# Performance work log

Measured on AMD Instinct MI355X. Metric: run time of the kernel, lower is better.

Reference implementation:

```python
import jax, jax.numpy as jnp
import numpy as np
from jax import lax

B, T, CIN, FN, H, W = 8, 8, 64, 64, 32, 32
GROUPS = 4 * FN // 32  # 8


def group_norm(x, g, b, groups, eps=1e-5):
    Bn, C, Hh, Ww = x.shape
    xr = x.reshape(Bn, groups, C // groups, Hh, Ww)
    mu = xr.mean(axis=(2, 3, 4), keepdims=True)
    var = xr.var(axis=(2, 3, 4), keepdims=True)
    xn = ((xr - mu) * lax.rsqrt(var + eps)).reshape(Bn, C, Hh, Ww)
    return xn * g[None, :, None, None] + b[None, :, None, None]


def conv1x1(x, w, b):
    # x: [B,C,H,W], w: [O,C]
    return jnp.einsum('bchw,oc->bohw', x, w) + b[None, :, None, None]


def setup_inputs() -> dict:
    key = jax.random.key(0)
    ks = jax.random.split(key, 8)
    s = 0.05
    return {
        'inputs': jax.random.normal(ks[0], (B, T, CIN, H, W), jnp.float32),
        'conv_w': jax.random.normal(ks[1], (4 * FN, CIN + FN, 3, 3), jnp.float32) * s,
        'conv_b': jnp.zeros((4 * FN,), jnp.float32),
        'gn_g': jnp.ones((4 * FN,), jnp.float32),
        'gn_b': jnp.zeros((4 * FN,), jnp.float32),
        'h_w': jax.random.normal(ks[2], (3 * FN, FN), jnp.float32) * s,
        'h_b': jnp.zeros((3 * FN,), jnp.float32),
        'm_w': jax.random.normal(ks[3], (2 * FN, FN), jnp.float32) * s,
        'm_b': jnp.zeros((2 * FN,), jnp.float32),
        'z1_w': jax.random.normal(ks[4], (FN, 2 * FN), jnp.float32) * s,
        'z1_b': jnp.zeros((FN,), jnp.float32),
        'z2_w': jax.random.normal(ks[5], (3 * FN, 2 * FN), jnp.float32) * s,
        'z2_b': jnp.zeros((3 * FN,), jnp.float32),
    }


def _sam(oh, im, h_w, h_b, m_w, m_b, z1_w, z1_b, z2_w, z2_b):
    Bn, C, Hh, Ww = oh.shape
    HW = Hh * Ww
    h_qkv = conv1x1(oh, h_w, h_b)  # [B,3C,H,W]
    m_kv = conv1x1(im, m_w, m_b)   # [B,2C,H,W]
    Qh, Kh, Vh = jnp.split(h_qkv, 3, axis=1)
    Km, Vm = jnp.split(m_kv, 2, axis=1)
    Q = Qh.reshape(Bn, C, HW).transpose(0, 2, 1)  # [B,HW,C]
    Kh = Kh.reshape(Bn, C, HW)
    Vh = Vh.reshape(Bn, C, HW)
    Km = Km.reshape(Bn, C, HW)
    Vm = Vm.reshape(Bn, C, HW)
    Ah = jax.nn.softmax(jnp.einsum('bnc,bcm->bnm', Q, Kh), axis=-1)  # [B,HW,HW]
    Am = jax.nn.softmax(jnp.einsum('bnc,bcm->bnm', Q, Km), axis=-1)
    Zh = jnp.einsum('bcn,bnm->bcm', Vh, Ah)  # [B,C,HW]
    Zm = jnp.einsum('bcn,bnm->bcm', Vm, Am)
    Zcat = jnp.concatenate([Zh, Zm], axis=1).reshape(Bn, 2 * C, Hh, Ww)
    Z = conv1x1(Zcat, z1_w, z1_b)  # [B,C,H,W]
    gates = conv1x1(jnp.concatenate([Z, oh], axis=1), z2_w, z2_b)  # [B,3C,H,W]
    o, g, i = jnp.split(gates, 3, axis=1)
    i = jax.nn.sigmoid(i)
    om = jnp.tanh(g) * i + (1.0 - i) * im
    oh2 = jax.nn.sigmoid(o) * om
    return oh2, om


def reference(inputs, conv_w, conv_b, gn_g, gn_b, h_w, h_b, m_w, m_b, z1_w, z1_b, z2_w, z2_b):
    Bn = inputs.shape[0]
    Hh, Ww = inputs.shape[-2], inputs.shape[-1]
    ih0 = jnp.zeros((Bn, FN, Hh, Ww), inputs.dtype)
    ic0 = jnp.zeros_like(ih0)
    im0 = jnp.zeros_like(ih0)

    def step(carry, x):
        ih, ic, im = carry
        comb = jnp.concatenate([x, ih], axis=1)
        gates = lax.conv_general_dilated(
            comb, conv_w, window_strides=(1, 1), padding='SAME',
            dimension_numbers=('NCHW', 'OIHW', 'NCHW')) + conv_b[None, :, None, None]
        gates = group_norm(gates, gn_g, gn_b, GROUPS)
        ingate, forgetgate, cellgate, outgate = jnp.split(gates, 4, axis=1)
        oc = ic * jax.nn.sigmoid(forgetgate) + jax.nn.sigmoid(ingate) * jnp.tanh(cellgate)
        oh = jax.nn.sigmoid(outgate) * jnp.tanh(oc)
        oh, om = _sam(oh, im, h_w, h_b, m_w, m_b, z1_w, z1_b, z2_w, z2_b)
        return (oh, oc, om), oh

    xs = jnp.moveaxis(inputs, 1, 0)  # [T,B,C,H,W]
    (ohT, ocT, imT), ys = lax.scan(step, (ih0, ic0, im0), xs)
    out = jnp.moveaxis(ys, 0, 1)  # [B,T,FN,H,W]
    return out, (ohT, ocT, imT)
```

## Files before the change

kernel.cpp:

```cpp
#include <hip/hip_runtime.h>
#include <math.h>


#define DEV __device__ __forceinline__

DEV float sigm(float x) { return 1.0f / (1.0f + __expf(-x)); }

DEV unsigned short f2bf(float f) {
  union { float f; unsigned u; } v; v.f = f;
  unsigned r = v.u + 0x7FFF + ((v.u >> 16) & 1);
  return (unsigned short)(r >> 16);
}

DEV unsigned pk2(float a, float b) {
  return (unsigned)f2bf(a) | ((unsigned)f2bf(b) << 16);
}

typedef float f32x4 __attribute__((ext_vector_type(4)));
typedef short bf16x8 __attribute__((ext_vector_type(8)));

__global__ __launch_bounds__(256) void wprep_kernel(
    const float* __restrict__ w, unsigned short* __restrict__ wpack)
{
  int e = blockIdx.x * 256 + threadIdx.x;
  int ci = e % 40;   int r = e / 40;
  int ocl = r % 128; r /= 128;
  int s = r % 36;    int oh = r / 36;
  int chh = s / 18;
  int t2  = s % 18;
  int tap = t2 >> 1, kc = t2 & 1;
  unsigned short v = 0;
  if (ci < 32) {
    int oc = oh * 128 + ocl;
    int c  = chh * 64 + kc * 32 + ci;
    v = f2bf(w[(size_t)(oc * 128 + c) * 9 + tap]);
  }
  wpack[e] = v;
}

__global__ __launch_bounds__(256) void wproj_kernel(
    const float* __restrict__ h_w, const float* __restrict__ m_w,
    const float* __restrict__ z1_w, const float* __restrict__ z2_w,
    unsigned short* __restrict__ wp)
{
  int e = blockIdx.x * 256 + threadIdx.x;
  if (e >= 53248) return;
  float v;
  if (e < 12288)       v = h_w[e];
  else if (e < 20480)  v = m_w[e - 12288];
  else if (e < 28672)  v = z1_w[e - 20480];
  else                 v = z2_w[e - 28672];
  wp[e] = f2bf(v);
}

__global__ __launch_bounds__(256) void conv3_mfma_kernel(
    const float* __restrict__ x,
    const float* __restrict__ ihb,
    const unsigned short* __restrict__ wpack,
    const float* __restrict__ bias,
    float* __restrict__ gates, int t)
{
  int ptile = blockIdx.x;
  int b     = blockIdx.y;
  int oh    = blockIdx.z;

  __shared__ __align__(16) unsigned short img[4 * 34 * 136];
  __shared__ __align__(16) unsigned short wbuf[2][128 * 40];

  int tid  = threadIdx.x;
  int lane = tid & 63;
  int wv   = tid >> 6;
  int mrow = wv >> 1, ncol = wv & 1;
  int y0 = ptile * 2;

  for (int i = tid; i < 4 * 34 * 136 / 2; i += 256) ((unsigned*)img)[i] = 0u;
  __syncthreads();

  const float* xsrc = x + (size_t)(b * 8 + t) * 65536;
  const float* hsrc = ihb + (size_t)b * 65536;
#pragma unroll
  for (int i = 0; i < 16; ++i) {
    int u = tid + i * 256;
    int ch = u >> 5;
    int v5 = u & 31;
    int row = v5 >> 3;
    int col4 = (v5 & 7) * 4;
    int gy = y0 - 1 + row;
    if (gy >= 0 && gy < 32) {
      const float* src = (ch < 64) ? (xsrc + (size_t)ch * 1024)
                                   : (hsrc + (size_t)(ch - 64) * 1024);
      float4 f = *(const float4*)(src + gy * 32 + col4);
      int base = (row * 34 + col4 + 1) * 136 + ch;
      img[base]       = f2bf(f.x);
      img[base + 136] = f2bf(f.y);
      img[base + 272] = f2bf(f.z);
      img[base + 408] = f2bf(f.w);
    }
  }

  const unsigned* wsl = (const unsigned*)wpack + (size_t)oh * 36 * 2560;
  unsigned* wb32 = (unsigned*)&wbuf[0][0];
#pragma unroll
  for (int k2 = 0; k2 < 10; ++k2)
    wb32[tid + k2 * 256] = wsl[tid + k2 * 256];
  __syncthreads();

  int aoff = (mrow * 64 + (lane & 15)) * 40 + (lane >> 4) * 8;
  int pb[2];
#pragma unroll
  for (int nf = 0; nf < 2; ++nf) {
    int pp = ncol * 32 + nf * 16 + (lane & 15);
    int rr = pp >> 5, cc = pp & 31;
    pb[nf] = (rr * 34 + cc) * 136 + (lane >> 4) * 8;
  }

  f32x4 acc[4][2] = {};
  unsigned wreg[10];

#pragma unroll
  for (int s = 0; s < 36; ++s) {
    int cur = s & 1;
    if (s < 35) {
      const unsigned* nsl = wsl + (s + 1) * 2560;
#pragma unroll
      for (int k2 = 0; k2 < 10; ++k2) wreg[k2] = nsl[tid + k2 * 256];
    }
    int chh = s / 18;
    int t2  = s % 18;
    int tap = t2 >> 1, kc = t2 & 1;
    int dy = tap / 3, dx = tap % 3;
    int toff = (dy * 34 + dx) * 136 + chh * 64 + kc * 32;

    bf16x8 a[4], bb[2];
#pragma unroll
    for (int mf = 0; mf < 4; ++mf)
      a[mf] = *(const bf16x8*)&wbuf[cur][aoff + mf * 640];
#pragma unroll
    for (int nf = 0; nf < 2; ++nf)
      bb[nf] = *(const bf16x8*)&img[pb[nf] + toff];
#pragma unroll
    for (int mf = 0; mf < 4; ++mf)
#pragma unroll
      for (int nf = 0; nf < 2; ++nf)
        acc[mf][nf] = __builtin_amdgcn_mfma_f32_16x16x32_bf16(
            a[mf], bb[nf], acc[mf][nf], 0, 0, 0);

    if (s < 35) {
      unsigned* dst = (unsigned*)&wbuf[0][0] + (1 - cur) * 2560;
#pragma unroll
      for (int k2 = 0; k2 < 10; ++k2) dst[tid + k2 * 256] = wreg[k2];
    }
    __syncthreads();
  }

  int orow_base = oh * 128 + mrow * 64 + (lane >> 4) * 4;
  int pcol = ptile * 64 + ncol * 32 + (lane & 15);
  float* gout = gates + (size_t)b * 262144;
#pragma unroll
  for (int mf = 0; mf < 4; ++mf)
#pragma unroll
    for (int nf = 0; nf < 2; ++nf)
#pragma unroll
      for (int r = 0; r < 4; ++r) {
        int oc_ = orow_base + mf * 16 + r;
        gout[(size_t)oc_ * 1024 + pcol + nf * 16] = acc[mf][nf][r] + bias[oc_];
      }
}

__global__ __launch_bounds__(256) void gnstats_kernel(
    const float* __restrict__ g, float* __restrict__ st)
{
  int grp = blockIdx.x; int b = blockIdx.y;
  const float* p0 = g + (size_t)b * 262144 + (size_t)grp * 32768;
  float s = 0.0f, q = 0.0f;
  for (int i = threadIdx.x; i < 8192; i += 256) {
    float4 a = *(const float4*)(p0 + (size_t)i * 4);
    s += a.x + a.y + a.z + a.w;
    q += a.x * a.x + a.y * a.y + a.z * a.z + a.w * a.w;
  }
#pragma unroll
  for (int off = 32; off > 0; off >>= 1) {
    s += __shfl_down(s, off);
    q += __shfl_down(q, off);
  }
  __shared__ float ss[4], qq[4];
  int wid = threadIdx.x >> 6;
  if ((threadIdx.x & 63) == 0) { ss[wid] = s; qq[wid] = q; }
  __syncthreads();
  if (threadIdx.x == 0) {
    float S = ss[0] + ss[1] + ss[2] + ss[3];
    float Q = qq[0] + qq[1] + qq[2] + qq[3];
    float mu = S / 32768.0f;
    float var = Q / 32768.0f - mu * mu;
    st[(b * 8 + grp) * 2]     = mu;
    st[(b * 8 + grp) * 2 + 1] = rsqrtf(var + 1e-5f);
  }
}

__global__ __launch_bounds__(256) void gnlstm_kernel(
    const float* __restrict__ g,
    const float* __restrict__ st, const float* __restrict__ gn_g,
    const float* __restrict__ gn_b, float* __restrict__ ic,
    float* __restrict__ cat2, float* __restrict__ out)
{
  int c = blockIdx.x; int b = blockIdx.y;
  int px = threadIdx.x * 4;
  size_t base = (size_t)b * 262144 + (size_t)c * 1024 + px;

  float4 vi4 = *(const float4*)(g + base);
  float4 vf4 = *(const float4*)(g + base + 65536);
  float4 vc4 = *(const float4*)(g + base + 131072);
  float4 vo4 = *(const float4*)(g + base + 196608);

  int ch0 = c, ch1 = 64 + c, ch2 = 128 + c, ch3 = 192 + c;
  float mu, is;
  mu = st[(b * 8 + (ch0 >> 5)) * 2]; is = st[(b * 8 + (ch0 >> 5)) * 2 + 1];
  float ga0 = gn_g[ch0] * is, bb0 = gn_b[ch0] - mu * ga0;
  mu = st[(b * 8 + (ch1 >> 5)) * 2]; is = st[(b * 8 + (ch1 >> 5)) * 2 + 1];
  float ga1 = gn_g[ch1] * is, bb1 = gn_b[ch1] - mu * ga1;
  mu = st[(b * 8 + (ch2 >> 5)) * 2]; is = st[(b * 8 + (ch2 >> 5)) * 2 + 1];
  float ga2 = gn_g[ch2] * is, bb2 = gn_b[ch2] - mu * ga2;
  mu = st[(b * 8 + (ch3 >> 5)) * 2]; is = st[(b * 8 + (ch3 >> 5)) * 2 + 1];
  float ga3 = gn_g[ch3] * is, bb3 = gn_b[ch3] - mu * ga3;

  size_t sb = (size_t)b * 65536 + (size_t)c * 1024 + px;
  float4 icv = *(const float4*)(ic + sb);
  float* vip = (float*)&vi4; float* vfp = (float*)&vf4;
  float* vcp = (float*)&vc4; float* vop = (float*)&vo4;
  float* icp = (float*)&icv;
  float4 ocv, ohv;
  float* ocp = (float*)&ocv; float* ohp = (float*)&ohv;
#pragma unroll
  for (int j = 0; j < 4; ++j) {
    float ing = sigm(vip[j] * ga0 + bb0);
    float fg  = sigm(vfp[j] * ga1 + bb1);
    float cg  = tanhf(vcp[j] * ga2 + bb2);
    float og  = sigm(vop[j] * ga3 + bb3);
    float oc  = icp[j] * fg + ing * cg;
    ocp[j] = oc;
    ohp[j] = og * tanhf(oc);
  }
  *(float4*)(ic + sb) = ocv;
  *(float4*)(out + 4718592 + sb) = ocv;
  *(float4*)(cat2 + (size_t)b * 131072 + (size_t)(64 + c) * 1024 + px) = ohv;
}

template <int K>
__global__ __launch_bounds__(256) void gemm_mfma_kernel(
    const unsigned short* __restrict__ Wp, const float* __restrict__ X,
    const float* __restrict__ X2, const float* __restrict__ bias,
    float* __restrict__ C, int xbs, int cbs)
{
  constexpr int KS = K + 8;
  constexpr int NKS = K / 32;
  int nt = blockIdx.x, mt = blockIdx.y, b = blockIdx.z;
  __shared__ __align__(16) unsigned short Xs[64 * KS];
  int tid = threadIdx.x, lane = tid & 63, w = tid >> 6;
  int n0 = nt * 64;
  const float* Xb  = X + (size_t)b * xbs;
  const float* X2b = X2 ? (X2 + (size_t)b * xbs) : nullptr;

#pragma unroll
  for (int i = 0; i < K / 8; ++i) {
    int u = tid + i * 256;
    int c2 = u >> 6, nl = u & 63;
    float f0 = Xb[(size_t)(2 * c2) * 1024 + n0 + nl];
    float f1 = Xb[(size_t)(2 * c2 + 1) * 1024 + n0 + nl];
    if (X2b) {
      f0 += X2b[(size_t)(2 * c2) * 1024 + n0 + nl];
      f1 += X2b[(size_t)(2 * c2 + 1) * 1024 + n0 + nl];
    }
    ((unsigned*)Xs)[nl * (KS / 2) + c2] = pk2(f0, f1);
  }
  __syncthreads();

  int mrow = mt * 64 + w * 16 + (lane & 15);
  bf16x8 ka[NKS];
#pragma unroll
  for (int ks = 0; ks < NKS; ++ks)
    ka[ks] = *(const bf16x8*)&Wp[(size_t)mrow * K + ks * 32 + (lane >> 4) * 8];

  f32x4 acc[4] = {};
#pragma unroll
  for (int nf = 0; nf < 4; ++nf) {
#pragma unroll
    for (int ks = 0; ks < NKS; ++ks) {
      bf16x8 bx = *(const bf16x8*)&Xs[(nf * 16 + (lane & 15)) * KS +
                                      ks * 32 + (lane >> 4) * 8];
      acc[nf] = __builtin_amdgcn_mfma_f32_16x16x32_bf16(ka[ks], bx, acc[nf], 0, 0, 0);
    }
  }

  float* Cb = C + (size_t)b * cbs;
#pragma unroll
  for (int nf = 0; nf < 4; ++nf)
#pragma unroll
    for (int r = 0; r < 4; ++r) {
      int m = mt * 64 + w * 16 + (lane >> 4) * 4 + r;
      Cb[(size_t)m * 1024 + n0 + nf * 16 + (lane & 15)] = acc[nf][r] + bias[m];
    }
}

__global__ __launch_bounds__(256) void att_stats_kernel(
    const float* __restrict__ qkv, const float* __restrict__ mkv,
    float* __restrict__ stats)
{
  int nt = blockIdx.x;
  int att = blockIdx.y >> 1, mh = blockIdx.y & 1;
  int b = blockIdx.z;
  const float* Qb = qkv + (size_t)b * 196608;
  const float* Kb = att ? (mkv + (size_t)b * 131072)
                        : (qkv + (size_t)b * 196608 + 65536);
  __shared__ __align__(16) unsigned short Qs[64 * 72];
  __shared__ __align__(16) unsigned short Ks[64 * 72];
  int tid = threadIdx.x, lane = tid & 63, w = tid >> 6;
  int n0 = nt * 64;

#pragma unroll
  for (int i = 0; i < 8; ++i) {
    int u = tid + i * 256;
    int c2 = u >> 6, nl = u & 63;
    float f0 = Qb[(size_t)(2 * c2) * 1024 + n0 + nl];
    float f1 = Qb[(size_t)(2 * c2 + 1) * 1024 + n0 + nl];
    ((unsigned*)Qs)[nl * 36 + c2] = pk2(f0, f1);
  }
  __syncthreads();
  bf16x8 qa0 = *(const bf16x8*)&Qs[(w * 16 + (lane & 15)) * 72 + (lane >> 4) * 8];
  bf16x8 qa1 = *(const bf16x8*)&Qs[(w * 16 + (lane & 15)) * 72 + 32 + (lane >> 4) * 8];

  float M[4] = {-3.0e38f, -3.0e38f, -3.0e38f, -3.0e38f};
  float Dsum[4] = {0.f, 0.f, 0.f, 0.f};

  for (int mt = mh * 8; mt < mh * 8 + 8; ++mt) {
    __syncthreads();
#pragma unroll
    for (int i = 0; i < 8; ++i) {
      int u = tid + i * 256;
      int c2 = u >> 6, ml = u & 63;
      float f0 = Kb[(size_t)(2 * c2) * 1024 + mt * 64 + ml];
      float f1 = Kb[(size_t)(2 * c2 + 1) * 1024 + mt * 64 + ml];
      ((unsigned*)Ks)[ml * 36 + c2] = pk2(f0, f1);
    }
    __syncthreads();
    f32x4 s[4];
#pragma unroll
    for (int mf = 0; mf < 4; ++mf) {
      bf16x8 b0 = *(const bf16x8*)&Ks[(mf * 16 + (lane & 15)) * 72 + (lane >> 4) * 8];
      bf16x8 b1 = *(const bf16x8*)&Ks[(mf * 16 + (lane & 15)) * 72 + 32 + (lane >> 4) * 8];
      f32x4 tacc = {};
      tacc = __builtin_amdgcn_mfma_f32_16x16x32_bf16(qa0, b0, tacc, 0, 0, 0);
      tacc = __builtin_amdgcn_mfma_f32_16x16x32_bf16(qa1, b1, tacc, 0, 0, 0);
      s[mf] = tacc;
    }
#pragma unroll
    for (int r = 0; r < 4; ++r) {
      float v0 = s[0][r], v1 = s[1][r], v2 = s[2][r], v3 = s[3][r];
      float mx = fmaxf(fmaxf(v0, v1), fmaxf(v2, v3));
      float nm = fmaxf(M[r], mx);
      Dsum[r] = Dsum[r] * __expf(M[r] - nm) +
                __expf(v0 - nm) + __expf(v1 - nm) +
                __expf(v2 - nm) + __expf(v3 - nm);
      M[r] = nm;
    }
  }
#pragma unroll
  for (int off = 1; off < 16; off <<= 1) {
#pragma unroll
    for (int r = 0; r < 4; ++r) {
      float Mo = __shfl_xor(M[r], off);
      float Do = __shfl_xor(Dsum[r], off);
      float nm = fmaxf(M[r], Mo);
      Dsum[r] = Dsum[r] * __expf(M[r] - nm) + Do * __expf(Mo - nm);
      M[r] = nm;
    }
  }
  if ((lane & 15) == 0) {
    float* stb = stats + (size_t)(((b * 2 + att) * 2 + mh) * 2) * 1024;
#pragma unroll
    for (int r = 0; r < 4; ++r) {
      int n = n0 + w * 16 + (lane >> 4) * 4 + r;
      stb[n] = M[r];
      stb[1024 + n] = Dsum[r];
    }
  }
}

__global__ __launch_bounds__(256) void att_z_kernel(
    const float* __restrict__ qkv, const float* __restrict__ mkv,
    const float* __restrict__ stats, float* __restrict__ zc0,
    float* __restrict__ zc1)
{
  int mt = blockIdx.x;
  int att = blockIdx.y >> 1, nh = blockIdx.y & 1;
  int b = blockIdx.z;
  const float* Qb = qkv + (size_t)b * 196608;
  const float* Kb = att ? (mkv + (size_t)b * 131072)
                        : (qkv + (size_t)b * 196608 + 65536);
  const float* Vb = att ? (mkv + (size_t)b * 131072 + 65536)
                        : (qkv + (size_t)b * 196608 + 131072);
  const float* stb = stats + (size_t)(b * 2 + att) * 4096;

  __shared__ __align__(16) unsigned short Ks[64 * 72];
  __shared__ __align__(16) unsigned short Qs[64 * 72];
  __shared__ __align__(16) unsigned short Vs[64 * 72];
  __shared__ __align__(16) unsigned short Ps[64 * 72];
  __shared__ float Mn[64];
  __shared__ float Rn[64];

  int tid = threadIdx.x, lane = tid & 63, w = tid >> 6;
  int m0 = mt * 64;

#pragma unroll
  for (int i = 0; i < 8; ++i) {
    int u = tid + i * 256;
    int c2 = u >> 6, ml = u & 63;
    float f0 = Kb[(size_t)(2 * c2) * 1024 + m0 + ml];
    float f1 = Kb[(size_t)(2 * c2 + 1) * 1024 + m0 + ml];
    ((unsigned*)Ks)[ml * 36 + c2] = pk2(f0, f1);
  }
  __syncthreads();
  bf16x8 bk[4][2];
#pragma unroll
  for (int mf = 0; mf < 4; ++mf) {
    bk[mf][0] = *(const bf16x8*)&Ks[(mf * 16 + (lane & 15)) * 72 + (lane >> 4) * 8];
    bk[mf][1] = *(const bf16x8*)&Ks[(mf * 16 + (lane & 15)) * 72 + 32 + (lane >> 4) * 8];
  }

  f32x4 zacc[4] = {};

  for (int ntb = nh * 8; ntb < nh * 8 + 8; ++ntb) {
    int n0 = ntb * 64;
    __syncthreads();
    if (tid < 64) {
      int n = n0 + tid;
      float M0 = stb[n],        D0 = stb[1024 + n];
      float M1 = stb[2048 + n], D1 = stb[3072 + n];
      float Mm = fmaxf(M0, M1);
      float Dm = D0 * __expf(M0 - Mm) + D1 * __expf(M1 - Mm);
      Mn[tid] = Mm;
      Rn[tid] = 1.0f / Dm;
    }
#pragma unroll
    for (int i = 0; i < 8; ++i) {
      int u = tid + i * 256;
      int c2 = u >> 6, nl = u & 63;
      float f0 = Qb[(size_t)(2 * c2) * 1024 + n0 + nl];
      float f1 = Qb[(size_t)(2 * c2 + 1) * 1024 + n0 + nl];
      ((unsigned*)Qs)[nl * 36 + c2] = pk2(f0, f1);
    }
    __syncthreads();
#pragma unroll
    for (int i = 0; i < 4; ++i) {
      int u = tid + i * 256;
      int c = u >> 4, n4 = (u & 15) * 4;
      float4 v = *(const float4*)(Vb + (size_t)c * 1024 + n0 + n4);
      unsigned* dst = (unsigned*)&Vs[c * 72 + n4];
      dst[0] = pk2(v.x * Rn[n4], v.y * Rn[n4 + 1]);
      dst[1] = pk2(v.z * Rn[n4 + 2], v.w * Rn[n4 + 3]);
    }

    bf16x8 qa0 = *(const bf16x8*)&Qs[(w * 16 + (lane & 15)) * 72 + (lane >> 4) * 8];
    bf16x8 qa1 = *(const bf16x8*)&Qs[(w * 16 + (lane & 15)) * 72 + 32 + (lane >> 4) * 8];
    float mr[4];
#pragma unroll
    for (int r = 0; r < 4; ++r) mr[r] = Mn[w * 16 + (lane >> 4) * 4 + r];
#pragma unroll
    for (int mf = 0; mf < 4; ++mf) {
      f32x4 tacc = {};
      tacc = __builtin_amdgcn_mfma_f32_16x16x32_bf16(qa0, bk[mf][0], tacc, 0, 0, 0);
      tacc = __builtin_amdgcn_mfma_f32_16x16x32_bf16(qa1, bk[mf][1], tacc, 0, 0, 0);
      unsigned* dst = (unsigned*)&Ps[(mf * 16 + (lane & 15)) * 72 +
                                     w * 16 + (lane >> 4) * 4];
      dst[0] = pk2(__expf(tacc[0] - mr[0]), __expf(tacc[1] - mr[1]));
      dst[1] = pk2(__expf(tacc[2] - mr[2]), __expf(tacc[3] - mr[3]));
    }
    __syncthreads();

    bf16x8 va0 = *(const bf16x8*)&Vs[(w * 16 + (lane & 15)) * 72 + (lane >> 4) * 8];
    bf16x8 va1 = *(const bf16x8*)&Vs[(w * 16 + (lane & 15)) * 72 + 32 + (lane >> 4) * 8];
#pragma unroll
    for (int mf = 0; mf < 4; ++mf) {
      bf16x8 p0 = *(const bf16x8*)&Ps[(mf * 16 + (lane & 15)) * 72 + (lane >> 4) * 8];
      bf16x8 p1 = *(const bf16x8*)&Ps[(mf * 16 + (lane & 15)) * 72 + 32 + (lane >> 4) * 8];
      zacc[mf] = __builtin_amdgcn_mfma_f32_16x16x32_bf16(va0, p0, zacc[mf], 0, 0, 0);
      zacc[mf] = __builtin_amdgcn_mfma_f32_16x16x32_bf16(va1, p1, zacc[mf], 0, 0, 0);
    }
  }

  float* zb = (nh ? zc1 : zc0) + (size_t)b * 131072 + (size_t)att * 65536;
#pragma unroll
  for (int mf = 0; mf < 4; ++mf)
#pragma unroll
    for (int r = 0; r < 4; ++r) {
      int c = w * 16 + (lane >> 4) * 4 + r;
      zb[(size_t)c * 1024 + m0 + mf * 16 + (lane & 15)] = zacc[mf][r];
    }
}

__global__ __launch_bounds__(256) void sam_kernel(
    const float* __restrict__ g2, float* __restrict__ im,
    float* __restrict__ ih, float* __restrict__ out, int t)
{
  int c = blockIdx.x; int b = blockIdx.y;
  int px = threadIdx.x * 4;
  size_t gb = (size_t)b * 196608 + (size_t)c * 1024 + px;
  float4 vo4 = *(const float4*)(g2 + gb);
  float4 vg4 = *(const float4*)(g2 + gb + 65536);
  float4 vi4 = *(const float4*)(g2 + gb + 131072);
  size_t sb = (size_t)b * 65536 + (size_t)c * 1024 + px;
  float4 vm4 = *(const float4*)(im + sb);
  float* vop = (float*)&vo4; float* vgp = (float*)&vg4;
  float* vip = (float*)&vi4; float* vmp = (float*)&vm4;
  float4 om4, oh4;
  float* omp = (float*)&om4; float* ohp = (float*)&oh4;
#pragma unroll
  for (int j = 0; j < 4; ++j) {
    float ig = sigm(vip[j]);
    float om = tanhf(vgp[j]) * ig + (1.0f - ig) * vmp[j];
    omp[j] = om;
    ohp[j] = sigm(vop[j]) * om;
  }
  *(float4*)(im + sb) = om4;
  *(float4*)(ih + sb) = oh4;
  *(float4*)(out + ((size_t)(b * 8 + t) * 64 + c) * 1024 + px) = oh4;
  *(float4*)(out + 4194304 + sb) = oh4;
  *(float4*)(out + 5242880 + sb) = om4;
}

extern "C" void kernel_launch(void* const* d_in, const int* in_sizes, int n_in,
                              void* d_out, int out_size, void* d_ws,
                              size_t ws_size, hipStream_t stream)
{
  const float* x      = (const float*)d_in[0];
  const float* conv_w = (const float*)d_in[1];
  const float* conv_b = (const float*)d_in[2];
  const float* gn_g   = (const float*)d_in[3];
  const float* gn_b   = (const float*)d_in[4];
  const float* h_w    = (const float*)d_in[5];
  const float* h_b    = (const float*)d_in[6];
  const float* m_w    = (const float*)d_in[7];
  const float* m_b    = (const float*)d_in[8];
  const float* z1_w   = (const float*)d_in[9];
  const float* z1_b   = (const float*)d_in[10];
  const float* z2_w   = (const float*)d_in[11];
  const float* z2_b   = (const float*)d_in[12];
  float* out = (float*)d_out;
  float* ws  = (float*)d_ws;

  float* ic     = ws;
  float* ih     = ws + 524288;
  float* im     = ws + 1048576;
  float* gates  = ws + 1572864;
  float* gnst   = ws + 3670016;
  float* qkv    = ws + 3670272;
  float* mkv    = ws + 5243136;
  float* stats  = ws + 6291712;
  float* cat2   = ws + 6357248;
  float* zc0    = ws + 7405824;
  unsigned short* wpack = (unsigned short*)(ws + 8454400);
  unsigned short* wproj = (unsigned short*)(ws + 8638720);
  float* zc1    = ws + 8665344;
  float* g2     = gates;

  const unsigned short* hp  = wproj;
  const unsigned short* mp  = wproj + 12288;
  const unsigned short* z1p = wproj + 20480;
  const unsigned short* z2p = wproj + 28672;

  hipMemsetAsync(ic, 0, (size_t)3 * 524288 * sizeof(float), stream);
  wprep_kernel<<<dim3(1440), 256, 0, stream>>>(conv_w, wpack);
  wproj_kernel<<<dim3(208), 256, 0, stream>>>(h_w, m_w, z1_w, z2_w, wproj);

  for (int t = 0; t < 8; ++t) {
    conv3_mfma_kernel<<<dim3(16, 8, 2), 256, 0, stream>>>(
        x, ih, wpack, conv_b, gates, t);
    gnstats_kernel<<<dim3(8, 8), 256, 0, stream>>>(gates, gnst);
    gnlstm_kernel<<<dim3(64, 8), 256, 0, stream>>>(gates, gnst, gn_g,
                                                   gn_b, ic, cat2, out);
    gemm_mfma_kernel<64><<<dim3(16, 3, 8), 256, 0, stream>>>(
        hp, cat2 + 65536, nullptr, h_b, qkv, 131072, 196608);
    gemm_mfma_kernel<64><<<dim3(16, 2, 8), 256, 0, stream>>>(
        mp, im, nullptr, m_b, mkv, 65536, 131072);
    att_stats_kernel<<<dim3(16, 4, 8), 256, 0, stream>>>(qkv, mkv, stats);
    att_z_kernel<<<dim3(16, 4, 8), 256, 0, stream>>>(qkv, mkv, stats, zc0, zc1);
    gemm_mfma_kernel<128><<<dim3(16, 1, 8), 256, 0, stream>>>(
        z1p, zc0, zc1, z1_b, cat2, 131072, 131072);
    gemm_mfma_kernel<128><<<dim3(16, 3, 8), 256, 0, stream>>>(
        z2p, cat2, nullptr, z2_b, g2, 131072, 196608);
    sam_kernel<<<dim3(64, 8), 256, 0, stream>>>(g2, im, ih, out, t);
  }
}
```

Measured before the change: 1.098 ms.

## Pre-pack attention Q/K/V to bf16 once and split attention z into quarters

Adds a pack kernel that converts Q, K and V to bf16 once per step, with Q and K transposed to a pixel-major layout. The attention stats and z kernels then read MFMA fragments straight from global memory instead of repeatedly converting fp32 tiles through shared memory. A separate kernel merges the two softmax-stat halves and precomputes the reciprocal. The z kernel's N range is split four ways for more parallelism, and the z1 GEMM sums the four partials. This adds two launches and extra workspace traffic in exchange for removing redundant conversions and barriers.

Measured after the change: 1.076 ms. 1.02x faster.

```diff
diff --git a/kernel.cpp b/kernel.cpp
--- a/kernel.cpp
+++ b/kernel.cpp
@@ -245,11 +245,10 @@
   *(float4*)(cat2 + (size_t)b * 131072 + (size_t)(64 + c) * 1024 + px) = ohv;
 }
 
-template <int K>
+template <int K, int NX>
 __global__ __launch_bounds__(256) void gemm_mfma_kernel(
     const unsigned short* __restrict__ Wp, const float* __restrict__ X,
-    const float* __restrict__ X2, const float* __restrict__ bias,
-    float* __restrict__ C, int xbs, int cbs)
+    const float* __restrict__ bias, float* __restrict__ C, int xbs, int cbs)
 {
   constexpr int KS = K + 8;
   constexpr int NKS = K / 32;
@@ -257,18 +256,19 @@
   __shared__ __align__(16) unsigned short Xs[64 * KS];
   int tid = threadIdx.x, lane = tid & 63, w = tid >> 6;
   int n0 = nt * 64;
-  const float* Xb  = X + (size_t)b * xbs;
-  const float* X2b = X2 ? (X2 + (size_t)b * xbs) : nullptr;
+  const float* Xb = X + (size_t)b * xbs;
 
 #pragma unroll
   for (int i = 0; i < K / 8; ++i) {
     int u = tid + i * 256;
     int c2 = u >> 6, nl = u & 63;
-    float f0 = Xb[(size_t)(2 * c2) * 1024 + n0 + nl];
-    float f1 = Xb[(size_t)(2 * c2 + 1) * 1024 + n0 + nl];
-    if (X2b) {
-      f0 += X2b[(size_t)(2 * c2) * 1024 + n0 + nl];
-      f1 += X2b[(size_t)(2 * c2 + 1) * 1024 + n0 + nl];
+    size_t i0 = (size_t)(2 * c2) * 1024 + n0 + nl;
+    size_t i1 = (size_t)(2 * c2 + 1) * 1024 + n0 + nl;
+    float f0 = Xb[i0], f1 = Xb[i1];
+#pragma unroll
+    for (int j = 1; j < NX; ++j) {
+      f0 += Xb[(size_t)j * 1048576 + i0];
+      f1 += Xb[(size_t)j * 1048576 + i1];
     }
     ((unsigned*)Xs)[nl * (KS / 2) + c2] = pk2(f0, f1);
   }
@@ -301,52 +301,79 @@
     }
 }
 
+__global__ __launch_bounds__(256) void attpack_kernel(
+    const float* __restrict__ qkv, const float* __restrict__ mkv,
+    unsigned short* __restrict__ apack)
+{
+  int nt = blockIdx.x, slab = blockIdx.y, b = blockIdx.z;
+  int tid = threadIdx.x;
+  int n0 = nt * 64;
+  const float* src;
+  if (slab == 0)      src = qkv + (size_t)b * 196608;
+  else if (slab == 1) src = qkv + (size_t)b * 196608 + 65536;
+  else if (slab == 2) src = mkv + (size_t)b * 131072;
+  else if (slab == 3) src = qkv + (size_t)b * 196608 + 131072;
+  else                src = mkv + (size_t)b * 131072 + 65536;
+  unsigned short* dst = apack + (size_t)slab * 524288 + (size_t)b * 65536;
+
+  if (slab < 3) {
+    __shared__ __align__(16) unsigned short T[64 * 72];
+#pragma unroll
+    for (int i = 0; i < 4; ++i) {
+      int u = tid + i * 256;
+      int c = u >> 4, n4 = (u & 15) * 4;
+      float4 f = *(const float4*)(src + (size_t)c * 1024 + n0 + n4);
+      T[(n4 + 0) * 72 + c] = f2bf(f.x);
+      T[(n4 + 1) * 72 + c] = f2bf(f.y);
+      T[(n4 + 2) * 72 + c] = f2bf(f.z);
+      T[(n4 + 3) * 72 + c] = f2bf(f.w);
+    }
+    __syncthreads();
+#pragma unroll
+    for (int i = 0; i < 8; ++i) {
+      int u = tid + i * 256;
+      int nl = u >> 5, c2 = u & 31;
+      ((unsigned*)dst)[(size_t)(n0 + nl) * 32 + c2] =
+          ((const unsigned*)T)[nl * 36 + c2];
+    }
+  } else {
+#pragma unroll
+    for (int i = 0; i < 4; ++i) {
+      int u = tid + i * 256;
+      int c = u >> 4, n4 = (u & 15) * 4;
+      float4 f = *(const float4*)(src + (size_t)c * 1024 + n0 + n4);
+      unsigned* d = (unsigned*)&dst[(size_t)c * 1024 + n0 + n4];
+      d[0] = pk2(f.x, f.y);
+      d[1] = pk2(f.z, f.w);
+    }
+  }
+}
+
 __global__ __launch_bounds__(256) void att_stats_kernel(
-    const float* __restrict__ qkv, const float* __restrict__ mkv,
-    float* __restrict__ stats)
+    const unsigned short* __restrict__ apack, float* __restrict__ stats)
 {
   int nt = blockIdx.x;
   int att = blockIdx.y >> 1, mh = blockIdx.y & 1;
   int b = blockIdx.z;
-  const float* Qb = qkv + (size_t)b * 196608;
-  const float* Kb = att ? (mkv + (size_t)b * 131072)
-                        : (qkv + (size_t)b * 196608 + 65536);
-  __shared__ __align__(16) unsigned short Qs[64 * 72];
-  __shared__ __align__(16) unsigned short Ks[64 * 72];
+  const unsigned short* Qtb = apack + (size_t)b * 65536;
+  const unsigned short* Ktb = apack + (size_t)(att ? 2 : 1) * 524288 +
+                              (size_t)b * 65536;
   int tid = threadIdx.x, lane = tid & 63, w = tid >> 6;
-  int n0 = nt * 64;
-
-#pragma unroll
-  for (int i = 0; i < 8; ++i) {
-    int u = tid + i * 256;
-    int c2 = u >> 6, nl = u & 63;
-    float f0 = Qb[(size_t)(2 * c2) * 1024 + n0 + nl];
-    float f1 = Qb[(size_t)(2 * c2 + 1) * 1024 + n0 + nl];
-    ((unsigned*)Qs)[nl * 36 + c2] = pk2(f0, f1);
-  }
-  __syncthreads();
-  bf16x8 qa0 = *(const bf16x8*)&Qs[(w * 16 + (lane & 15)) * 72 + (lane >> 4) * 8];
-  bf16x8 qa1 = *(const bf16x8*)&Qs[(w * 16 + (lane & 15)) * 72 + 32 + (lane >> 4) * 8];
+  int l15 = lane & 15, lh = lane >> 4;
+  int nq = nt * 64 + w * 16 + l15;
+  bf16x8 qa0 = *(const bf16x8*)&Qtb[(size_t)nq * 64 + lh * 8];
+  bf16x8 qa1 = *(const bf16x8*)&Qtb[(size_t)nq * 64 + 32 + lh * 8];
 
   float M[4] = {-3.0e38f, -3.0e38f, -3.0e38f, -3.0e38f};
   float Dsum[4] = {0.f, 0.f, 0.f, 0.f};
 
   for (int mt = mh * 8; mt < mh * 8 + 8; ++mt) {
-    __syncthreads();
-#pragma unroll
-    for (int i = 0; i < 8; ++i) {
-      int u = tid + i * 256;
-      int c2 = u >> 6, ml = u & 63;
-      float f0 = Kb[(size_t)(2 * c2) * 1024 + mt * 64 + ml];
-      float f1 = Kb[(size_t)(2 * c2 + 1) * 1024 + mt * 64 + ml];
-      ((unsigned*)Ks)[ml * 36 + c2] = pk2(f0, f1);
-    }
-    __syncthreads();
     f32x4 s[4];
 #pragma unroll
     for (int mf = 0; mf < 4; ++mf) {
-      bf16x8 b0 = *(const bf16x8*)&Ks[(mf * 16 + (lane & 15)) * 72 + (lane >> 4) * 8];
-      bf16x8 b1 = *(const bf16x8*)&Ks[(mf * 16 + (lane & 15)) * 72 + 32 + (lane >> 4) * 8];
+      int m = mt * 64 + mf * 16 + l15;
+      bf16x8 b0 = *(const bf16x8*)&Ktb[(size_t)m * 64 + lh * 8];
+      bf16x8 b1 = *(const bf16x8*)&Ktb[(size_t)m * 64 + 32 + lh * 8];
       f32x4 tacc = {};
       tacc = __builtin_amdgcn_mfma_f32_16x16x32_bf16(qa0, b0, tacc, 0, 0, 0);
       tacc = __builtin_amdgcn_mfma_f32_16x16x32_bf16(qa1, b1, tacc, 0, 0, 0);
@@ -374,126 +401,108 @@
       M[r] = nm;
     }
   }
-  if ((lane & 15) == 0) {
+  if (l15 == 0) {
     float* stb = stats + (size_t)(((b * 2 + att) * 2 + mh) * 2) * 1024;
 #pragma unroll
     for (int r = 0; r < 4; ++r) {
-      int n = n0 + w * 16 + (lane >> 4) * 4 + r;
+      int n = nt * 64 + w * 16 + lh * 4 + r;
       stb[n] = M[r];
       stb[1024 + n] = Dsum[r];
     }
   }
 }
 
+__global__ __launch_bounds__(256) void statmerge_kernel(
+    const float* __restrict__ stats, float* __restrict__ stats2)
+{
+  int i = blockIdx.x * 256 + threadIdx.x;
+  int n = i & 1023, ba = i >> 10;
+  const float* stb = stats + (size_t)ba * 4096;
+  float M0 = stb[n], D0 = stb[1024 + n];
+  float M1 = stb[2048 + n], D1 = stb[3072 + n];
+  float Mm = fmaxf(M0, M1);
+  float R = 1.0f / (D0 * __expf(M0 - Mm) + D1 * __expf(M1 - Mm));
+  stats2[(size_t)ba * 2048 + n] = Mm;
+  stats2[(size_t)ba * 2048 + 1024 + n] = R;
+}
+
 __global__ __launch_bounds__(256) void att_z_kernel(
-    const float* __restrict__ qkv, const float* __restrict__ mkv,
-    const float* __restrict__ stats, float* __restrict__ zc0,
-    float* __restrict__ zc1)
+    const unsigned short* __restrict__ apack,
+    const float* __restrict__ stats2, float* __restrict__ zc)
 {
   int mt = blockIdx.x;
-  int att = blockIdx.y >> 1, nh = blockIdx.y & 1;
+  int att = blockIdx.y >> 2, nh = blockIdx.y & 3;
   int b = blockIdx.z;
-  const float* Qb = qkv + (size_t)b * 196608;
-  const float* Kb = att ? (mkv + (size_t)b * 131072)
-                        : (qkv + (size_t)b * 196608 + 65536);
-  const float* Vb = att ? (mkv + (size_t)b * 131072 + 65536)
-                        : (qkv + (size_t)b * 196608 + 131072);
-  const float* stb = stats + (size_t)(b * 2 + att) * 4096;
-
-  __shared__ __align__(16) unsigned short Ks[64 * 72];
-  __shared__ __align__(16) unsigned short Qs[64 * 72];
-  __shared__ __align__(16) unsigned short Vs[64 * 72];
+  const unsigned short* Qtb = apack + (size_t)b * 65536;
+  const unsigned short* Ktb = apack + (size_t)(att ? 2 : 1) * 524288 +
+                              (size_t)b * 65536;
+  const unsigned short* Vtb = apack + (size_t)(att ? 4 : 3) * 524288 +
+                              (size_t)b * 65536;
+  const float* stM = stats2 + (size_t)(b * 2 + att) * 2048;
+  const float* stR = stM + 1024;
+
   __shared__ __align__(16) unsigned short Ps[64 * 72];
-  __shared__ float Mn[64];
-  __shared__ float Rn[64];
 
   int tid = threadIdx.x, lane = tid & 63, w = tid >> 6;
+  int l15 = lane & 15, lh = lane >> 4;
   int m0 = mt * 64;
 
-#pragma unroll
-  for (int i = 0; i < 8; ++i) {
-    int u = tid + i * 256;
-    int c2 = u >> 6, ml = u & 63;
-    float f0 = Kb[(size_t)(2 * c2) * 1024 + m0 + ml];
-    float f1 = Kb[(size_t)(2 * c2 + 1) * 1024 + m0 + ml];
-    ((unsigned*)Ks)[ml * 36 + c2] = pk2(f0, f1);
-  }
-  __syncthreads();
   bf16x8 bk[4][2];
 #pragma unroll
   for (int mf = 0; mf < 4; ++mf) {
-    bk[mf][0] = *(const bf16x8*)&Ks[(mf * 16 + (lane & 15)) * 72 + (lane >> 4) * 8];
-    bk[mf][1] = *(const bf16x8*)&Ks[(mf * 16 + (lane & 15)) * 72 + 32 + (lane >> 4) * 8];
+    int m = m0 + mf * 16 + l15;
+    bk[mf][0] = *(const bf16x8*)&Ktb[(size_t)m * 64 + lh * 8];
+    bk[mf][1] = *(const bf16x8*)&Ktb[(size_t)m * 64 + 32 + lh * 8];
   }
 
   f32x4 zacc[4] = {};
 
-  for (int ntb = nh * 8; ntb < nh * 8 + 8; ++ntb) {
+  for (int ntb = nh * 4; ntb < nh * 4 + 4; ++ntb) {
     int n0 = ntb * 64;
-    __syncthreads();
-    if (tid < 64) {
-      int n = n0 + tid;
-      float M0 = stb[n],        D0 = stb[1024 + n];
-      float M1 = stb[2048 + n], D1 = stb[3072 + n];
-      float Mm = fmaxf(M0, M1);
-      float Dm = D0 * __expf(M0 - Mm) + D1 * __expf(M1 - Mm);
-      Mn[tid] = Mm;
-      Rn[tid] = 1.0f / Dm;
-    }
-#pragma unroll
-    for (int i = 0; i < 8; ++i) {
-      int u = tid + i * 256;
-      int c2 = u >> 6, nl = u & 63;
-      float f0 = Qb[(size_t)(2 * c2) * 1024 + n0 + nl];
-      float f1 = Qb[(size_t)(2 * c2 + 1) * 1024 + n0 + nl];
-      ((unsigned*)Qs)[nl * 36 + c2] = pk2(f0, f1);
-    }
-    __syncthreads();
-#pragma unroll
-    for (int i = 0; i < 4; ++i) {
-      int u = tid + i * 256;
-      int c = u >> 4, n4 = (u & 15) * 4;
-      float4 v = *(const float4*)(Vb + (size_t)c * 1024 + n0 + n4);
-      unsigned* dst = (unsigned*)&Vs[c * 72 + n4];
-      dst[0] = pk2(v.x * Rn[n4], v.y * Rn[n4 + 1]);
-      dst[1] = pk2(v.z * Rn[n4 + 2], v.w * Rn[n4 + 3]);
-    }
-
-    bf16x8 qa0 = *(const bf16x8*)&Qs[(w * 16 + (lane & 15)) * 72 + (lane >> 4) * 8];
-    bf16x8 qa1 = *(const bf16x8*)&Qs[(w * 16 + (lane & 15)) * 72 + 32 + (lane >> 4) * 8];
-    float mr[4];
-#pragma unroll
-    for (int r = 0; r < 4; ++r) mr[r] = Mn[w * 16 + (lane >> 4) * 4 + r];
+    int nq = n0 + w * 16 + l15;
+    bf16x8 qa0 = *(const bf16x8*)&Qtb[(size_t)nq * 64 + lh * 8];
+    bf16x8 qa1 = *(const bf16x8*)&Qtb[(size_t)nq * 64 + 32 + lh * 8];
+    float mr[4], rr[4];
+#pragma unroll
+    for (int r = 0; r < 4; ++r) {
+      int n = n0 + w * 16 + lh * 4 + r;
+      mr[r] = stM[n];
+      rr[r] = stR[n];
+    }
 #pragma unroll
     for (int mf = 0; mf < 4; ++mf) {
       f32x4 tacc = {};
       tacc = __builtin_amdgcn_mfma_f32_16x16x32_bf16(qa0, bk[mf][0], tacc, 0, 0, 0);
       tacc = __builtin_amdgcn_mfma_f32_16x16x32_bf16(qa1, bk[mf][1], tacc, 0, 0, 0);
-      unsigned* dst = (unsigned*)&Ps[(mf * 16 + (lane & 15)) * 72 +
-                                     w * 16 + (lane >> 4) * 4];
-      dst[0] = pk2(__expf(tacc[0] - mr[0]), __expf(tacc[1] - mr[1]));
-      dst[1] = pk2(__expf(tacc[2] - mr[2]), __expf(tacc[3] - mr[3]));
+      unsigned* dst = (unsigned*)&Ps[(mf * 16 + l15) * 72 + w * 16 + lh * 4];
+      dst[0] = pk2(__expf(tacc[0] - mr[0]) * rr[0],
+                   __expf(tacc[1] - mr[1]) * rr[1]);
+      dst[1] = pk2(__expf(tacc[2] - mr[2]) * rr[2],
+                   __expf(tacc[3] - mr[3]) * rr[3]);
     }
     __syncthreads();
 
-    bf16x8 va0 = *(const bf16x8*)&Vs[(w * 16 + (lane & 15)) * 72 + (lane >> 4) * 8];
-    bf16x8 va1 = *(const bf16x8*)&Vs[(w * 16 + (lane & 15)) * 72 + 32 + (lane >> 4) * 8];
+    int cv = w * 16 + l15;
+    bf16x8 va0 = *(const bf16x8*)&Vtb[(size_t)cv * 1024 + n0 + lh * 8];
+    bf16x8 va1 = *(const bf16x8*)&Vtb[(size_t)cv * 1024 + n0 + 32 + lh * 8];
 #pragma unroll
     for (int mf = 0; mf < 4; ++mf) {
-      bf16x8 p0 = *(const bf16x8*)&Ps[(mf * 16 + (lane & 15)) * 72 + (lane >> 4) * 8];
-      bf16x8 p1 = *(const bf16x8*)&Ps[(mf * 16 + (lane & 15)) * 72 + 32 + (lane >> 4) * 8];
+      bf16x8 p0 = *(const bf16x8*)&Ps[(mf * 16 + l15) * 72 + lh * 8];
+      bf16x8 p1 = *(const bf16x8*)&Ps[(mf * 16 + l15) * 72 + 32 + lh * 8];
       zacc[mf] = __builtin_amdgcn_mfma_f32_16x16x32_bf16(va0, p0, zacc[mf], 0, 0, 0);
       zacc[mf] = __builtin_amdgcn_mfma_f32_16x16x32_bf16(va1, p1, zacc[mf], 0, 0, 0);
     }
-  }
-
-  float* zb = (nh ? zc1 : zc0) + (size_t)b * 131072 + (size_t)att * 65536;
+    __syncthreads();
+  }
+
+  float* zb = zc + (size_t)nh * 1048576 + (size_t)b * 131072 +
+              (size_t)att * 65536;
 #pragma unroll
   for (int mf = 0; mf < 4; ++mf)
 #pragma unroll
     for (int r = 0; r < 4; ++r) {
-      int c = w * 16 + (lane >> 4) * 4 + r;
-      zb[(size_t)c * 1024 + m0 + mf * 16 + (lane & 15)] = zacc[mf][r];
+      int c = w * 16 + lh * 4 + r;
+      zb[(size_t)c * 1024 + m0 + mf * 16 + l15] = zacc[mf][r];
     }
 }
 
@@ -556,10 +565,11 @@
   float* mkv    = ws + 5243136;
   float* stats  = ws + 6291712;
   float* cat2   = ws + 6357248;
-  float* zc0    = ws + 7405824;
-  unsigned short* wpack = (unsigned short*)(ws + 8454400);
-  unsigned short* wproj = (unsigned short*)(ws + 8638720);
-  float* zc1    = ws + 8665344;
+  float* stats2 = ws + 7405824;
+  unsigned short* wpack = (unsigned short*)(ws + 7438592);
+  unsigned short* wproj = (unsigned short*)(ws + 7622912);
+  unsigned short* apack = (unsigned short*)(ws + 7649536);
+  float* zc     = ws + 8960256;
   float* g2     = gates;
 
   const unsigned short* hp  = wproj;
@@ -577,16 +587,18 @@
     gnstats_kernel<<<dim3(8, 8), 256, 0, stream>>>(gates, gnst);
     gnlstm_kernel<<<dim3(64, 8), 256, 0, stream>>>(gates, gnst, gn_g,
                                                    gn_b, ic, cat2, out);
-    gemm_mfma_kernel<64><<<dim3(16, 3, 8), 256, 0, stream>>>(
-        hp, cat2 + 65536, nullptr, h_b, qkv, 131072, 196608);
-    gemm_mfma_kernel<64><<<dim3(16, 2, 8), 256, 0, stream>>>(
-        mp, im, nullptr, m_b, mkv, 65536, 131072);
-    att_stats_kernel<<<dim3(16, 4, 8), 256, 0, stream>>>(qkv, mkv, stats);
-    att_z_kernel<<<dim3(16, 4, 8), 256, 0, stream>>>(qkv, mkv, stats, zc0, zc1);
-    gemm_mfma_kernel<128><<<dim3(16, 1, 8), 256, 0, stream>>>(
-        z1p, zc0, zc1, z1_b, cat2, 131072, 131072);
-    gemm_mfma_kernel<128><<<dim3(16, 3, 8), 256, 0, stream>>>(
-        z2p, cat2, nullptr, z2_b, g2, 131072, 196608);
+    gemm_mfma_kernel<64, 1><<<dim3(16, 3, 8), 256, 0, stream>>>(
+        hp, cat2 + 65536, h_b, qkv, 131072, 196608);
+    gemm_mfma_kernel<64, 1><<<dim3(16, 2, 8), 256, 0, stream>>>(
+        mp, im, m_b, mkv, 65536, 131072);
+    attpack_kernel<<<dim3(16, 5, 8), 256, 0, stream>>>(qkv, mkv, apack);
+    att_stats_kernel<<<dim3(16, 4, 8), 256, 0, stream>>>(apack, stats);
+    statmerge_kernel<<<dim3(64), 256, 0, stream>>>(stats, stats2);
+    att_z_kernel<<<dim3(16, 8, 8), 256, 0, stream>>>(apack, stats2, zc);
+    gemm_mfma_kernel<128, 4><<<dim3(16, 1, 8), 256, 0, stream>>>(
+        z1p, zc, z1_b, cat2, 131072, 131072);
+    gemm_mfma_kernel<128, 1><<<dim3(16, 3, 8), 256, 0, stream>>>(
+        z2p, cat2, z2_b, g2, 131072, 196608);
     sam_kernel<<<dim3(64, 8), 256, 0, stream>>>(g2, im, ih, out, t);
   }
 }
```
